# Performance work log

Measured on AMD Instinct MI355X. Metric: run time of the kernel, lower is better.

The kernel has to match this reference:

```python
import jax, jax.numpy as jnp
import numpy as np
from jax import lax

B, S, C = 32, 4096, 512   # batch, seq_len, input_dim
P, K = 3, 10              # pairs_per_fan_in, max_fan_in


def setup_inputs() -> dict:
    key = jax.random.key(0)
    keys = jax.random.split(key, K + 1)
    inp = {"x": jax.random.normal(keys[0], (B, S, C), dtype=jnp.float32)}
    for k in range(1, K + 1):
        # WIO layout: (kernel_width=k, in_channels=C, out_channels=P)
        fan_in = C * k
        scale = 1.0 / np.sqrt(fan_in)  # kaiming-uniform-ish scale
        inp[f"w{k}"] = scale * jax.random.normal(keys[k], (k, C, P), dtype=jnp.float32)
    return inp


def _causal_conv(x, w):
    # x: (B, S, C), w: (k, C, P) -> (B, S, P); left-pad k-1 == torch padding=k-1 then [:, :, :S]
    k = w.shape[0]
    return lax.conv_general_dilated(
        x, w, window_strides=(1,), padding=[(k - 1, 0)],
        dimension_numbers=("NWC", "WIO", "NWC"))


def reference(x, w1, w2, w3, w4, w5, w6, w7, w8, w9, w10) -> jnp.ndarray:
    ws = (w1, w2, w3, w4, w5, w6, w7, w8, w9, w10)
    # ReLU each causal conv output, concat along feature dim -> (B, S, K*P)
    parts = [jax.nn.relu(_causal_conv(x, w)) for w in ws]
    return jnp.concatenate(parts, axis=-1)
```

## Files before the change

kernel.cpp:

```cpp
#include <hip/hip_runtime.h>

typedef _Float16 half8 __attribute__((ext_vector_type(8)));
typedef _Float16 half4 __attribute__((ext_vector_type(4)));
typedef __attribute__((ext_vector_type(4))) float f32x4;

#define C_DIM 512
#define S_DIM 4096
#define NCOL 165
#define NCOLP 176
#define LDK 40
#define M_OUT 64
#define BK 32
#define NCHUNK 16
#define YST 180
#define YSLOT 2880

struct WP { const float* w[10]; };

__global__ __launch_bounds__(256) void prep_kernel(WP wp, _Float16* bt) {
  int idx = blockIdx.x * 256 + threadIdx.x;
  int col = idx >> 9;
  int c = idx & 511;
  float v = 0.f;
  if (col < NCOL) {
    int kw = 1, base = 0;
    while (col >= base + 3 * kw) { base += 3 * kw; ++kw; }
    int rem = col - base;
    int t = rem / 3, p = rem - 3 * t;
    v = wp.w[kw - 1][(t * C_DIM + c) * 3 + p];
  }
  bt[col * C_DIM + c] = (_Float16)v;
}

__device__ __forceinline__ void barrier_lgkm() {
  __asm__ volatile("s_waitcnt lgkmcnt(0)\n\ts_barrier" ::: "memory");
}

__global__ __launch_bounds__(256, 4) void conv_kernel(const float* __restrict__ x,
                                                      const _Float16* __restrict__ bt,
                                                      float* __restrict__ out) {
  __shared__ __align__(16) unsigned char smem[23040];
  float* Ys = (float*)smem;

  const int tid = threadIdx.x;
  const int b = blockIdx.x >> 6;
  const int tile = blockIdx.x & 63;
  const int s0 = tile * M_OUT;
  const int sBase = s0 - 16;
  const int wave = tid >> 6;
  const int lane = tid & 63;
  const int lane15 = lane & 15;
  const int quad = lane >> 4;
  const int n0 = wave * 3;
  const int nmine = (wave < 3) ? 3 : 2;

  const half8* bptr[3];
#pragma unroll
  for (int nn = 0; nn < 3; ++nn) {
    int cr = (n0 + nn) * 16 + lane15;
    bptr[nn] = (const half8*)&bt[(nn < nmine ? cr : lane15) * C_DIM + quad * 8];
  }

  const float4* aptr[3];
  bool aexists[3], avalid[3];
  int arow[3], aq[3];
#pragma unroll
  for (int i = 0; i < 3; ++i) {
    int idx = tid + i * 256;
    aexists[i] = (idx < 640);
    arow[i] = idx >> 3;
    aq[i] = idx & 7;
    int s = sBase + arow[i];
    avalid[i] = aexists[i] && (s >= 0);
    aptr[i] = (const float4*)&x[((size_t)(b * S_DIM + (s < 0 ? 0 : s))) * C_DIM + aq[i] * 4];
  }

  float4 pf[3];
  half8 bcur[3], bnxt[3];
  f32x4 acc[5][3];
#pragma unroll
  for (int m = 0; m < 5; ++m)
#pragma unroll
    for (int n = 0; n < 3; ++n) acc[m][n] = (f32x4){0.f, 0.f, 0.f, 0.f};

  auto loadA = [&](int ch) {
#pragma unroll
    for (int i = 0; i < 3; ++i) {
      if (avalid[i]) pf[i] = aptr[i][ch * 8];
      else pf[i] = make_float4(0.f, 0.f, 0.f, 0.f);
    }
  };
  auto cvtWrite = [&](int buf) {
    _Float16* Ah = (_Float16*)(smem + buf * 6400);
#pragma unroll
    for (int i = 0; i < 3; ++i) {
      if (aexists[i]) {
        half4 h = {(_Float16)pf[i].x, (_Float16)pf[i].y,
                   (_Float16)pf[i].z, (_Float16)pf[i].w};
        *(half4*)&Ah[arow[i] * LDK + aq[i] * 4] = h;
      }
    }
  };

  loadA(0);
  cvtWrite(0);
#pragma unroll
  for (int nn = 0; nn < 3; ++nn)
    if (nn < nmine) bcur[nn] = bptr[nn][0];
  loadA(1);
  barrier_lgkm();

#pragma unroll
  for (int ch = 0; ch < NCHUNK; ++ch) {
    if (ch < NCHUNK - 1) {
#pragma unroll
      for (int nn = 0; nn < 3; ++nn)
        if (nn < nmine) bnxt[nn] = bptr[nn][(ch + 1) * 4];
    }
    const _Float16* Ah = (const _Float16*)(smem + (ch & 1) * 6400);
#pragma unroll
    for (int m = 0; m < 5; ++m) {
      half8 a = *(const half8*)&Ah[(m * 16 + lane15) * LDK + quad * 8];
#pragma unroll
      for (int nn = 0; nn < 3; ++nn)
        if (nn < nmine)
          acc[m][nn] = __builtin_amdgcn_mfma_f32_16x16x32_f16(a, bcur[nn], acc[m][nn], 0, 0, 0);
    }
    if (ch < NCHUNK - 1) {
      cvtWrite((ch + 1) & 1);
      if (ch < NCHUNK - 2) loadA(ch + 2);
#pragma unroll
      for (int nn = 0; nn < 3; ++nn)
        if (nn < nmine) bcur[nn] = bnxt[nn];
    }
    barrier_lgkm();
  }

#pragma unroll
  for (int i = 1; i <= 4; ++i) {
    if (i == 1) {
#pragma unroll
      for (int nn = 0; nn < 3; ++nn)
        if (nn < nmine)
#pragma unroll
          for (int r = 0; r < 4; ++r)
            Ys[0 * YSLOT + (quad * 4 + r) * YST + (n0 + nn) * 16 + lane15] = acc[0][nn][r];
    }
#pragma unroll
    for (int nn = 0; nn < 3; ++nn)
      if (nn < nmine)
#pragma unroll
        for (int r = 0; r < 4; ++r)
          Ys[(i & 1) * YSLOT + (quad * 4 + r) * YST + (n0 + nn) * 16 + lane15] = acc[i][nn][r];
    __syncthreads();
    for (int o = tid; o < 480; o += 256) {
      int r = o / 30;
      int j = o - 30 * r;
      int kw = j / 3 + 1;
      int p = j - (kw - 1) * 3;
      int base = 3 * (kw * (kw - 1)) / 2;
      float sum = 0.f;
      for (int d = 0; d < kw; ++d) {
        int rr = r - d;
        int slot = (rr >= 0) ? (i & 1) : ((i ^ 1) & 1);
        int lr = (rr >= 0) ? rr : (16 + rr);
        int colv = base + (kw - 1 - d) * 3 + p;
        sum += Ys[slot * YSLOT + lr * YST + colv];
      }
      int s = s0 + 16 * (i - 1) + r;
      out[((size_t)(b * S_DIM + s)) * 30 + j] = fmaxf(sum, 0.f);
    }
    __syncthreads();
  }
}

extern "C" void kernel_launch(void* const* d_in, const int* in_sizes, int n_in,
                              void* d_out, int out_size, void* d_ws, size_t ws_size,
                              hipStream_t stream) {
  const float* x = (const float*)d_in[0];
  WP wp;
  for (int k = 0; k < 10; ++k) wp.w[k] = (const float*)d_in[k + 1];
  _Float16* bt = (_Float16*)d_ws;
  prep_kernel<<<NCOLP * C_DIM / 256, 256, 0, stream>>>(wp, bt);
  conv_kernel<<<32 * (S_DIM / M_OUT), 256, 0, stream>>>(x, bt, (float*)d_out);
}
```

Measured before the change: 417.5 us.

## Stream x tiles directly to LDS with global_load_lds and triple buffering

Replaces register-staged global loads plus fp16 conversion and LDS writes with direct global-to-LDS 16-byte loads into a three-deep fp32 buffer. The fp16 conversion moves to the LDS read side just before the MFMA. Out-of-range rows read from a zeroed workspace buffer that the prep kernel now fills. The goal is to free registers and VALU work and to overlap loads better. In exchange it doubles LDS traffic because tiles are stored as fp32, and it drops the occupancy hint from 4 to 3.

```diff
diff --git a/kernel.cpp b/kernel.cpp
--- a/kernel.cpp
+++ b/kernel.cpp
@@ -1,23 +1,28 @@
 #include <hip/hip_runtime.h>
 
 typedef _Float16 half8 __attribute__((ext_vector_type(8)));
-typedef _Float16 half4 __attribute__((ext_vector_type(4)));
 typedef __attribute__((ext_vector_type(4))) float f32x4;
 
 #define C_DIM 512
 #define S_DIM 4096
 #define NCOL 165
 #define NCOLP 176
-#define LDK 40
 #define M_OUT 64
+#define ROWS 80
 #define BK 32
 #define NCHUNK 16
+#define RJ 9
+#define BUFSZ 12288
 #define YST 180
 #define YSLOT 2880
 
 struct WP { const float* w[10]; };
 
-__global__ __launch_bounds__(256) void prep_kernel(WP wp, _Float16* bt) {
+__global__ __launch_bounds__(256) void prep_kernel(WP wp, _Float16* bt, float4* zbuf) {
+  if (blockIdx.x == NCOLP * C_DIM / 256) {
+    zbuf[threadIdx.x] = make_float4(0.f, 0.f, 0.f, 0.f);
+    return;
+  }
   int idx = blockIdx.x * 256 + threadIdx.x;
   int col = idx >> 9;
   int c = idx & 511;
@@ -32,14 +37,24 @@
   bt[col * C_DIM + c] = (_Float16)v;
 }
 
+__device__ __forceinline__ void gld16(const void* g, void* l) {
+  __builtin_amdgcn_global_load_lds(
+      (const __attribute__((address_space(1))) unsigned int*)(const unsigned int*)g,
+      (__attribute__((address_space(3))) unsigned int*)(unsigned int*)l, 16, 0, 0);
+}
+
+__device__ __forceinline__ void wait_vm3() {
+  __asm__ volatile("s_waitcnt vmcnt(3)" ::: "memory");
+}
 __device__ __forceinline__ void barrier_lgkm() {
   __asm__ volatile("s_waitcnt lgkmcnt(0)\n\ts_barrier" ::: "memory");
 }
 
-__global__ __launch_bounds__(256, 4) void conv_kernel(const float* __restrict__ x,
+__global__ __launch_bounds__(256, 3) void conv_kernel(const float* __restrict__ x,
                                                       const _Float16* __restrict__ bt,
+                                                      const float* __restrict__ zbuf,
                                                       float* __restrict__ out) {
-  __shared__ __align__(16) unsigned char smem[23040];
+  __shared__ __align__(16) unsigned char smem[3 * BUFSZ];
   float* Ys = (float*)smem;
 
   const int tid = threadIdx.x;
@@ -49,92 +64,79 @@
   const int sBase = s0 - 16;
   const int wave = tid >> 6;
   const int lane = tid & 63;
-  const int lane15 = lane & 15;
+  const int l15 = lane & 15;
   const int quad = lane >> 4;
+  const int wnu = __builtin_amdgcn_readfirstlane(wave);
   const int n0 = wave * 3;
   const int nmine = (wave < 3) ? 3 : 2;
 
   const half8* bptr[3];
 #pragma unroll
   for (int nn = 0; nn < 3; ++nn) {
-    int cr = (n0 + nn) * 16 + lane15;
-    bptr[nn] = (const half8*)&bt[(nn < nmine ? cr : lane15) * C_DIM + quad * 8];
+    int cr = (n0 + nn) * 16 + l15;
+    bptr[nn] = (const half8*)&bt[(nn < nmine ? cr : l15) * C_DIM + quad * 8];
   }
 
-  const float4* aptr[3];
-  bool aexists[3], avalid[3];
-  int arow[3], aq[3];
+  const char* asrc[3];
 #pragma unroll
   for (int i = 0; i < 3; ++i) {
-    int idx = tid + i * 256;
-    aexists[i] = (idx < 640);
-    arow[i] = idx >> 3;
-    aq[i] = idx & 7;
-    int s = sBase + arow[i];
-    avalid[i] = aexists[i] && (s >= 0);
-    aptr[i] = (const float4*)&x[((size_t)(b * S_DIM + (s < 0 ? 0 : s))) * C_DIM + aq[i] * 4];
+    int t = wave * 3 + i;
+    int sigma = t * 64 + lane;
+    int row = sigma / RJ;
+    int j = sigma - row * RJ;
+    int s = sBase + row;
+    bool ok = (j < 8) && (row < ROWS) && (s >= 0);
+    asrc[i] = ok ? (const char*)&x[((size_t)(b * S_DIM + s)) * C_DIM + j * 4]
+                 : (const char*)zbuf + lane * 16;
   }
+  const int ldst = wnu * 3;
 
-  float4 pf[3];
-  half8 bcur[3], bnxt[3];
   f32x4 acc[5][3];
 #pragma unroll
   for (int m = 0; m < 5; ++m)
 #pragma unroll
     for (int n = 0; n < 3; ++n) acc[m][n] = (f32x4){0.f, 0.f, 0.f, 0.f};
 
-  auto loadA = [&](int ch) {
 #pragma unroll
-    for (int i = 0; i < 3; ++i) {
-      if (avalid[i]) pf[i] = aptr[i][ch * 8];
-      else pf[i] = make_float4(0.f, 0.f, 0.f, 0.f);
-    }
-  };
-  auto cvtWrite = [&](int buf) {
-    _Float16* Ah = (_Float16*)(smem + buf * 6400);
+  for (int i = 0; i < 3; ++i)
+    gld16(asrc[i], smem + (ldst + i) * 1024);
 #pragma unroll
-    for (int i = 0; i < 3; ++i) {
-      if (aexists[i]) {
-        half4 h = {(_Float16)pf[i].x, (_Float16)pf[i].y,
-                   (_Float16)pf[i].z, (_Float16)pf[i].w};
-        *(half4*)&Ah[arow[i] * LDK + aq[i] * 4] = h;
-      }
-    }
-  };
-
-  loadA(0);
-  cvtWrite(0);
-#pragma unroll
-  for (int nn = 0; nn < 3; ++nn)
-    if (nn < nmine) bcur[nn] = bptr[nn][0];
-  loadA(1);
+  for (int i = 0; i < 3; ++i)
+    gld16(asrc[i] + 128, smem + BUFSZ + (ldst + i) * 1024);
+  wait_vm3();
   barrier_lgkm();
 
 #pragma unroll
   for (int ch = 0; ch < NCHUNK; ++ch) {
-    if (ch < NCHUNK - 1) {
+    const int cb = ch % 3;
+    const int nb = (ch + 2) % 3;
+    half8 bfr[3];
 #pragma unroll
-      for (int nn = 0; nn < 3; ++nn)
-        if (nn < nmine) bnxt[nn] = bptr[nn][(ch + 1) * 4];
+    for (int nn = 0; nn < 3; ++nn)
+      if (nn < nmine) bfr[nn] = bptr[nn][ch * 4];
+    if (ch < NCHUNK - 2) {
+#pragma unroll
+      for (int i = 0; i < 3; ++i)
+        gld16(asrc[i] + (ch + 2) * 128, smem + nb * BUFSZ + (ldst + i) * 1024);
     }
-    const _Float16* Ah = (const _Float16*)(smem + (ch & 1) * 6400);
+    const float* Af = (const float*)(smem + cb * BUFSZ);
 #pragma unroll
     for (int m = 0; m < 5; ++m) {
-      half8 a = *(const half8*)&Ah[(m * 16 + lane15) * LDK + quad * 8];
+      const float* rp = Af + (m * 16 + l15) * (RJ * 4) + quad * 8;
+      f32x4 a0 = *(const f32x4*)rp;
+      f32x4 a1 = *(const f32x4*)(rp + 4);
+      half8 ah = {(_Float16)a0[0], (_Float16)a0[1], (_Float16)a0[2], (_Float16)a0[3],
+                  (_Float16)a1[0], (_Float16)a1[1], (_Float16)a1[2], (_Float16)a1[3]};
 #pragma unroll
       for (int nn = 0; nn < 3; ++nn)
         if (nn < nmine)
-          acc[m][nn] = __builtin_amdgcn_mfma_f32_16x16x32_f16(a, bcur[nn], acc[m][nn], 0, 0, 0);
+          acc[m][nn] = __builtin_amdgcn_mfma_f32_16x16x32_f16(ah, bfr[nn], acc[m][nn], 0, 0, 0);
     }
-    if (ch < NCHUNK - 1) {
-      cvtWrite((ch + 1) & 1);
-      if (ch < NCHUNK - 2) loadA(ch + 2);
-#pragma unroll
-      for (int nn = 0; nn < 3; ++nn)
-        if (nn < nmine) bcur[nn] = bnxt[nn];
-    }
+    wait_vm3();
     barrier_lgkm();
   }
+
+  __syncthreads();
 
 #pragma unroll
   for (int i = 1; i <= 4; ++i) {
@@ -144,14 +146,14 @@
         if (nn < nmine)
 #pragma unroll
           for (int r = 0; r < 4; ++r)
-            Ys[0 * YSLOT + (quad * 4 + r) * YST + (n0 + nn) * 16 + lane15] = acc[0][nn][r];
+            Ys[0 * YSLOT + (quad * 4 + r) * YST + (n0 + nn) * 16 + l15] = acc[0][nn][r];
     }
 #pragma unroll
     for (int nn = 0; nn < 3; ++nn)
       if (nn < nmine)
 #pragma unroll
         for (int r = 0; r < 4; ++r)
-          Ys[(i & 1) * YSLOT + (quad * 4 + r) * YST + (n0 + nn) * 16 + lane15] = acc[i][nn][r];
+          Ys[(i & 1) * YSLOT + (quad * 4 + r) * YST + (n0 + nn) * 16 + l15] = acc[i][nn][r];
     __syncthreads();
     for (int o = tid; o < 480; o += 256) {
       int r = o / 30;
@@ -181,6 +183,8 @@
   WP wp;
   for (int k = 0; k < 10; ++k) wp.w[k] = (const float*)d_in[k + 1];
   _Float16* bt = (_Float16*)d_ws;
-  prep_kernel<<<NCOLP * C_DIM / 256, 256, 0, stream>>>(wp, bt);
-  conv_kernel<<<32 * (S_DIM / M_OUT), 256, 0, stream>>>(x, bt, (float*)d_out);
+  float4* zbuf = (float4*)((char*)d_ws + NCOLP * C_DIM * 2);
+  prep_kernel<<<NCOLP * C_DIM / 256 + 1, 256, 0, stream>>>(wp, bt, zbuf);
+  conv_kernel<<<32 * (S_DIM / M_OUT), 256, 0, stream>>>(x, bt, (const float*)zbuf,
+                                                        (float*)d_out);
 }
```

Result: faster. 407.1 us (-2.5%).
